# Kernel tuning notes

Measured on AMD Instinct MI355X. Metric: run time of the kernel, lower is better.

## Reference

```python
import jax, jax.numpy as jnp
import numpy as np

N_NODES = 100000


def gcn_conv(x, src, dst, w, W, b, n):
    # PyG GCNConv: add self loops (weight 1), symmetric normalization,
    # linear transform, scatter-add aggregation, bias.
    loop = jnp.arange(n, dtype=src.dtype)
    s = jnp.concatenate([src, loop])
    d = jnp.concatenate([dst, loop])
    ew = jnp.concatenate([w, jnp.ones((n,), dtype=w.dtype)])
    deg = jax.ops.segment_sum(ew, d, num_segments=n)          # [N]
    dinv = jnp.where(deg > 0, jax.lax.rsqrt(deg), 0.0).astype(x.dtype)
    norm = dinv[s] * ew * dinv[d]                             # [E+N]
    h = x @ W                                                 # [N, out]
    msg = h[s] * norm[:, None]                                # gather + scale
    out = jax.ops.segment_sum(msg, d, num_segments=n)         # scatter-add
    return out + b


def setup_inputs() -> dict:
    key = jax.random.key(0)
    k1, k2, k3, k4, k5, k6 = jax.random.split(key, 6)
    n, e, c_in, c_hid, c_out = N_NODES, 1200000, 64, 64, 32
    node_matrix = jax.random.normal(k1, (n, c_in), dtype=jnp.float32)
    edge_index = jax.random.randint(k2, (2, e), 0, n, dtype=jnp.int64)
    edge_weights = jax.random.uniform(k3, (e,), dtype=jnp.float32)
    s_in = 1.0 / np.sqrt(c_in)
    s_hid = 1.0 / np.sqrt(c_hid)
    W1 = jax.random.uniform(k4, (c_in, c_hid), jnp.float32, -s_in, s_in)
    b1 = jnp.zeros((c_hid,), jnp.float32)
    W2 = jax.random.uniform(k5, (c_hid, c_out), jnp.float32, -s_hid, s_hid)
    b2 = jnp.zeros((c_out,), jnp.float32)
    return {"node_matrix": node_matrix, "edge_index": edge_index,
            "edge_weights": edge_weights, "W1": W1, "b1": b1, "W2": W2, "b2": b2}


def reference(node_matrix, edge_index, edge_weights, W1, b1, W2, b2):
    n = node_matrix.shape[0]
    src, dst = edge_index[0], edge_index[1]
    x = gcn_conv(node_matrix, src, dst, edge_weights, W1, b1, n)
    x = jax.nn.relu(x)
    x = gcn_conv(x, src, dst, edge_weights, W2, b2, n)
    return x
```

## Files before the change

### kernel.cpp

```cpp
#include <hip/hip_runtime.h>

static inline int ceil_div(long long a, long long b) { return (int)((a + b - 1) / b); }

#define RBITS 8
#define RNODES 256
#define CNT_BLOCKS 96

typedef __attribute__((ext_vector_type(8))) short bf16x8;
typedef __attribute__((ext_vector_type(4))) float f32x4;

__device__ inline unsigned f2bf(float f) {
    unsigned u = __float_as_uint(f);
    return (u + 0x7fffu + ((u >> 16) & 1u)) >> 16;
}
__device__ inline unsigned pack2(float a, float b) { return f2bf(a) | (f2bf(b) << 16); }
__device__ inline float bf2f(unsigned v) { return __uint_as_float(v << 16); }
__device__ inline float bf_lo(unsigned v) { return __uint_as_float(v << 16); }
__device__ inline float bf_hi(unsigned v) { return __uint_as_float(v & 0xffff0000u); }

__global__ void bin_count(const int* __restrict__ dst, int* __restrict__ hist_g,
                          int NB, int E) {
    __shared__ int hist[512];
    int t = threadIdx.x;
    hist[t] = 0;
    __syncthreads();
    int nvec = E >> 2;
    const int4* d4 = (const int4*)dst;
    for (int v = blockIdx.x * 512 + t; v < nvec; v += CNT_BLOCKS * 512) {
        int4 d = d4[v];
        atomicAdd(&hist[d.x >> RBITS], 1);
        atomicAdd(&hist[d.y >> RBITS], 1);
        atomicAdd(&hist[d.z >> RBITS], 1);
        atomicAdd(&hist[d.w >> RBITS], 1);
    }
    if (blockIdx.x == 0 && t < (E & 3))
        atomicAdd(&hist[dst[(nvec << 2) + t] >> RBITS], 1);
    __syncthreads();
    if (t < NB) hist_g[blockIdx.x * NB + t] = hist[t];
}

__global__ void bin_scan(const int* __restrict__ hist_g, int* __restrict__ bin_start,
                         int* __restrict__ bin_cursor, int NB) {
    __shared__ int s[512];
    int t = threadIdx.x;
    int v = 0;
    if (t < NB) {
        for (int k = 0; k < CNT_BLOCKS; ++k) v += hist_g[k * NB + t];
        bin_cursor[t] = 0;
    }
    s[t] = v;
    __syncthreads();
    for (int d = 1; d < 512; d <<= 1) {
        int a = (t >= d) ? s[t - d] : 0;
        __syncthreads();
        s[t] += a;
        __syncthreads();
    }
    if (t < NB) bin_start[t] = s[t] - v;
    if (t == NB - 1) bin_start[NB] = s[t];
}

#define SC_T 512
#define SC_K 8
#define SC_E (SC_T * SC_K)
__global__ void bin_scatter(const int* __restrict__ src, const int* __restrict__ dst,
                            const float* __restrict__ w, int* __restrict__ bin_cursor,
                            const int* __restrict__ bin_start,
                            int* __restrict__ bp, float* __restrict__ bw,
                            int NB, int E) {
    __shared__ int hist[512];
    __shared__ int offs[512];
    __shared__ int base[512];
    __shared__ int stage_p[SC_E];
    __shared__ float stage_w[SC_E];
    __shared__ unsigned short stage_b[SC_E];
    int t = threadIdx.x;
    hist[t] = 0;
    __syncthreads();
    int e0 = blockIdx.x * SC_E;
    int nE = E - e0; if (nE > SC_E) nE = SC_E;

    int myBin[SC_K], myRank[SC_K], myPack[SC_K];
    float myW[SC_K];
#pragma unroll
    for (int k = 0; k < SC_K; ++k) {
        int idx = t + k * SC_T;
        if (idx < nE) {
            int e = e0 + idx;
            int d = dst[e];
            int b = d >> RBITS;
            myBin[k] = b;
            myPack[k] = (src[e] << RBITS) | (d & (RNODES - 1));
            myW[k] = w[e];
            myRank[k] = atomicAdd(&hist[b], 1);
        }
    }
    __syncthreads();
    offs[t] = hist[t];
    __syncthreads();
    for (int d = 1; d < 512; d <<= 1) {
        int a = (t >= d) ? offs[t - d] : 0;
        __syncthreads();
        offs[t] += a;
        __syncthreads();
    }
    if (t < NB && hist[t]) base[t] = bin_start[t] + atomicAdd(&bin_cursor[t], hist[t]);
#pragma unroll
    for (int k = 0; k < SC_K; ++k) {
        int idx = t + k * SC_T;
        if (idx < nE) {
            int b = myBin[k];
            int pos = (offs[b] - hist[b]) + myRank[k];
            stage_p[pos] = myPack[k];
            stage_w[pos] = myW[k];
            stage_b[pos] = (unsigned short)b;
        }
    }
    __syncthreads();
    for (int p = t; p < nE; p += SC_T) {
        int b = stage_b[p];
        int g = base[b] + (p - (offs[b] - hist[b]));
        bp[g] = stage_p[p];
        bw[g] = stage_w[p];
    }
}

__global__ void deg_csr(const int* __restrict__ bp, const float* __restrict__ bw,
                        const int* __restrict__ bin_start,
                        int* __restrict__ row_beg, int* __restrict__ row_cnt,
                        float* __restrict__ dinv, int N) {
    __shared__ int cnt[RNODES];
    __shared__ float wsum[RNODES];
    __shared__ int starts[RNODES];
    int b = blockIdx.x;
    int t = threadIdx.x;
    if (t < RNODES) { cnt[t] = 0; wsum[t] = 0.f; }
    __syncthreads();
    int beg = bin_start[b], end = bin_start[b + 1];
    for (int e = beg + t; e < end; e += 512) {
        int off = bp[e] & (RNODES - 1);
        atomicAdd(&cnt[off], 1);
        atomicAdd(&wsum[off], bw[e]);
    }
    __syncthreads();
    if (t < RNODES) starts[t] = cnt[t];
    __syncthreads();
    for (int d = 1; d < RNODES; d <<= 1) {
        int a = 0;
        if (t < RNODES && t >= d) a = starts[t - d];
        __syncthreads();
        if (t < RNODES) starts[t] += a;
        __syncthreads();
    }
    if (t < RNODES) {
        int node = (b << RBITS) + t;
        if (node < N) {
            row_beg[node] = beg + (starts[t] - cnt[t]);
            row_cnt[node] = cnt[t];
            dinv[node] = rsqrtf(wsum[t] + 1.0f);
        }
    }
}

__global__ void csr_scatter(const int* __restrict__ bp, const float* __restrict__ bw,
                            const int* __restrict__ bin_start, const int* __restrict__ row_beg,
                            const float* __restrict__ dinv, uint2* __restrict__ ew, int N) {
    __shared__ int cur[RNODES];
    int b = blockIdx.x;
    int t = threadIdx.x;
    if (t < RNODES) {
        int node = (b << RBITS) + t;
        cur[t] = (node < N) ? row_beg[node] : 0;
    }
    __syncthreads();
    int beg = bin_start[b], end = bin_start[b + 1];
    for (int e = beg + t; e < end; e += 512) {
        int p = bp[e];
        int s = p >> RBITS;
        int slot = atomicAdd(&cur[p & (RNODES - 1)], 1);
        uint2 v;
        v.x = (unsigned)s;
        v.y = __float_as_uint(bw[e] * dinv[s]);
        ew[slot] = v;
    }
}

__global__ __launch_bounds__(256) void gemm1_mfma(const float* __restrict__ X,
                                                  const float* __restrict__ W,
                                                  unsigned short* __restrict__ H, int N) {
    int lane = threadIdx.x & 63;
    int wv = threadIdx.x >> 6;
    int quad = lane >> 4;
    int col = lane & 15;

    bf16x8 Bh[4][2], Bl[4][2];
#pragma unroll
    for (int nt = 0; nt < 4; ++nt)
#pragma unroll
        for (int kh = 0; kh < 2; ++kh)
#pragma unroll
            for (int j = 0; j < 8; ++j) {
                float wval = W[(kh * 32 + quad * 8 + j) * 64 + nt * 16 + col];
                unsigned hb = f2bf(wval);
                Bh[nt][kh][j] = (short)hb;
                Bl[nt][kh][j] = (short)f2bf(wval - bf2f(hb));
            }

#pragma unroll
    for (int rt = 0; rt < 4; ++rt) {
        int rb = blockIdx.x * 256 + wv * 64 + rt * 16;
        if (rb >= N) break;
        int arow = rb + col;
        bf16x8 Ah[2], Al[2];
#pragma unroll
        for (int kh = 0; kh < 2; ++kh) {
            float xv[8];
            if (arow < N) {
                const float4* p = (const float4*)(X + (size_t)arow * 64 + kh * 32 + quad * 8);
                float4 f0 = p[0], f1 = p[1];
                xv[0] = f0.x; xv[1] = f0.y; xv[2] = f0.z; xv[3] = f0.w;
                xv[4] = f1.x; xv[5] = f1.y; xv[6] = f1.z; xv[7] = f1.w;
            } else {
#pragma unroll
                for (int j = 0; j < 8; ++j) xv[j] = 0.f;
            }
#pragma unroll
            for (int j = 0; j < 8; ++j) {
                unsigned hb = f2bf(xv[j]);
                Ah[kh][j] = (short)hb;
                Al[kh][j] = (short)f2bf(xv[j] - bf2f(hb));
            }
        }
        f32x4 acc[4] = {{0,0,0,0},{0,0,0,0},{0,0,0,0},{0,0,0,0}};
#pragma unroll
        for (int nt = 0; nt < 4; ++nt)
#pragma unroll
            for (int kh = 0; kh < 2; ++kh) {
                acc[nt] = __builtin_amdgcn_mfma_f32_16x16x32_bf16(Ah[kh], Bh[nt][kh], acc[nt], 0, 0, 0);
                acc[nt] = __builtin_amdgcn_mfma_f32_16x16x32_bf16(Al[kh], Bh[nt][kh], acc[nt], 0, 0, 0);
                acc[nt] = __builtin_amdgcn_mfma_f32_16x16x32_bf16(Ah[kh], Bl[nt][kh], acc[nt], 0, 0, 0);
            }
#pragma unroll
        for (int nt = 0; nt < 4; ++nt)
#pragma unroll
            for (int r = 0; r < 4; ++r) {
                int row = rb + quad * 4 + r;
                if (row < N)
                    H[(size_t)row * 64 + nt * 16 + col] = (unsigned short)f2bf(acc[nt][r]);
            }
    }
}

__global__ __launch_bounds__(256) void gemm2_mfma(const unsigned short* __restrict__ Xb,
                                                  const float* __restrict__ W,
                                                  unsigned short* __restrict__ H, int N) {
    int lane = threadIdx.x & 63;
    int wv = threadIdx.x >> 6;
    int quad = lane >> 4;
    int col = lane & 15;

    bf16x8 Bh[2][2], Bl[2][2];
#pragma unroll
    for (int nt = 0; nt < 2; ++nt)
#pragma unroll
        for (int kh = 0; kh < 2; ++kh)
#pragma unroll
            for (int j = 0; j < 8; ++j) {
                float wval = W[(kh * 32 + quad * 8 + j) * 32 + nt * 16 + col];
                unsigned hb = f2bf(wval);
                Bh[nt][kh][j] = (short)hb;
                Bl[nt][kh][j] = (short)f2bf(wval - bf2f(hb));
            }

#pragma unroll
    for (int rt = 0; rt < 4; ++rt) {
        int rb = blockIdx.x * 256 + wv * 64 + rt * 16;
        if (rb >= N) break;
        int arow = rb + col;
        bf16x8 A[2];
#pragma unroll
        for (int kh = 0; kh < 2; ++kh) {
            if (arow < N) {
                const bf16x8* p = (const bf16x8*)(Xb + (size_t)arow * 64 + kh * 32 + quad * 8);
                A[kh] = *p;
            } else {
                A[kh] = bf16x8{0,0,0,0,0,0,0,0};
            }
        }
        f32x4 acc[2] = {{0,0,0,0},{0,0,0,0}};
#pragma unroll
        for (int nt = 0; nt < 2; ++nt)
#pragma unroll
            for (int kh = 0; kh < 2; ++kh) {
                acc[nt] = __builtin_amdgcn_mfma_f32_16x16x32_bf16(A[kh], Bh[nt][kh], acc[nt], 0, 0, 0);
                acc[nt] = __builtin_amdgcn_mfma_f32_16x16x32_bf16(A[kh], Bl[nt][kh], acc[nt], 0, 0, 0);
            }
#pragma unroll
        for (int nt = 0; nt < 2; ++nt)
#pragma unroll
            for (int r = 0; r < 4; ++r) {
                int row = rb + quad * 4 + r;
                if (row < N)
                    H[(size_t)row * 32 + nt * 16 + col] = (unsigned short)f2bf(acc[nt][r]);
            }
    }
}

__global__ void aggregate64(const unsigned* __restrict__ h, const int* __restrict__ row_beg,
                            const int* __restrict__ row_cnt, const uint2* __restrict__ ew,
                            const float* __restrict__ dinv, const float* __restrict__ b,
                            unsigned* __restrict__ outb, int N) {
    int t = threadIdx.x;
    int c = t & 7;
    int i = blockIdx.x * 64 + (t >> 3);
    if (i >= N) return;
    int e = row_beg[i];
    int end = e + row_cnt[i];
    const uint4* h4 = (const uint4*)h;
    float acc[8];
#pragma unroll
    for (int j = 0; j < 8; ++j) acc[j] = 0.f;
    for (; e + 3 < end; e += 4) {
        uint2 e0 = ew[e], e1 = ew[e + 1], e2 = ew[e + 2], e3 = ew[e + 3];
        float n0 = __uint_as_float(e0.y);
        float n1 = __uint_as_float(e1.y);
        float n2 = __uint_as_float(e2.y);
        float n3 = __uint_as_float(e3.y);
        uint4 v0 = h4[(size_t)e0.x * 8 + c];
        uint4 v1 = h4[(size_t)e1.x * 8 + c];
        uint4 v2 = h4[(size_t)e2.x * 8 + c];
        uint4 v3 = h4[(size_t)e3.x * 8 + c];
        acc[0] += n0 * bf_lo(v0.x) + n1 * bf_lo(v1.x) + n2 * bf_lo(v2.x) + n3 * bf_lo(v3.x);
        acc[1] += n0 * bf_hi(v0.x) + n1 * bf_hi(v1.x) + n2 * bf_hi(v2.x) + n3 * bf_hi(v3.x);
        acc[2] += n0 * bf_lo(v0.y) + n1 * bf_lo(v1.y) + n2 * bf_lo(v2.y) + n3 * bf_lo(v3.y);
        acc[3] += n0 * bf_hi(v0.y) + n1 * bf_hi(v1.y) + n2 * bf_hi(v2.y) + n3 * bf_hi(v3.y);
        acc[4] += n0 * bf_lo(v0.z) + n1 * bf_lo(v1.z) + n2 * bf_lo(v2.z) + n3 * bf_lo(v3.z);
        acc[5] += n0 * bf_hi(v0.z) + n1 * bf_hi(v1.z) + n2 * bf_hi(v2.z) + n3 * bf_hi(v3.z);
        acc[6] += n0 * bf_lo(v0.w) + n1 * bf_lo(v1.w) + n2 * bf_lo(v2.w) + n3 * bf_lo(v3.w);
        acc[7] += n0 * bf_hi(v0.w) + n1 * bf_hi(v1.w) + n2 * bf_hi(v2.w) + n3 * bf_hi(v3.w);
    }
    for (; e < end; ++e) {
        uint2 e0 = ew[e];
        float n0 = __uint_as_float(e0.y);
        uint4 v0 = h4[(size_t)e0.x * 8 + c];
        acc[0] += n0 * bf_lo(v0.x);
        acc[1] += n0 * bf_hi(v0.x);
        acc[2] += n0 * bf_lo(v0.y);
        acc[3] += n0 * bf_hi(v0.y);
        acc[4] += n0 * bf_lo(v0.z);
        acc[5] += n0 * bf_hi(v0.z);
        acc[6] += n0 * bf_lo(v0.w);
        acc[7] += n0 * bf_hi(v0.w);
    }
    float di = dinv[i];
    uint4 hv = h4[(size_t)i * 8 + c];
    float hs[8] = {bf_lo(hv.x), bf_hi(hv.x), bf_lo(hv.y), bf_hi(hv.y),
                   bf_lo(hv.z), bf_hi(hv.z), bf_lo(hv.w), bf_hi(hv.w)};
    float4 b0 = ((const float4*)b)[c * 2];
    float4 b1 = ((const float4*)b)[c * 2 + 1];
    float o[8];
    o[0] = b0.x + di * (di * hs[0] + acc[0]);
    o[1] = b0.y + di * (di * hs[1] + acc[1]);
    o[2] = b0.z + di * (di * hs[2] + acc[2]);
    o[3] = b0.w + di * (di * hs[3] + acc[3]);
    o[4] = b1.x + di * (di * hs[4] + acc[4]);
    o[5] = b1.y + di * (di * hs[5] + acc[5]);
    o[6] = b1.z + di * (di * hs[6] + acc[6]);
    o[7] = b1.w + di * (di * hs[7] + acc[7]);
#pragma unroll
    for (int j = 0; j < 8; ++j) o[j] = fmaxf(o[j], 0.f);
    uint4 ov;
    ov.x = pack2(o[0], o[1]);
    ov.y = pack2(o[2], o[3]);
    ov.z = pack2(o[4], o[5]);
    ov.w = pack2(o[6], o[7]);
    ((uint4*)outb)[(size_t)i * 8 + c] = ov;
}

__global__ void aggregate32(const unsigned* __restrict__ h, const int* __restrict__ row_beg,
                            const int* __restrict__ row_cnt, const uint2* __restrict__ ew,
                            const float* __restrict__ dinv, const float* __restrict__ b,
                            float* __restrict__ out, int N) {
    int t = threadIdx.x;
    int c = t & 3;
    int i = blockIdx.x * 128 + (t >> 2);
    if (i >= N) return;
    int e = row_beg[i];
    int end = e + row_cnt[i];
    const uint4* h4 = (const uint4*)h;
    float acc[8];
#pragma unroll
    for (int j = 0; j < 8; ++j) acc[j] = 0.f;
    for (; e + 3 < end; e += 4) {
        uint2 e0 = ew[e], e1 = ew[e + 1], e2 = ew[e + 2], e3 = ew[e + 3];
        float n0 = __uint_as_float(e0.y);
        float n1 = __uint_as_float(e1.y);
        float n2 = __uint_as_float(e2.y);
        float n3 = __uint_as_float(e3.y);
        uint4 v0 = h4[(size_t)e0.x * 4 + c];
        uint4 v1 = h4[(size_t)e1.x * 4 + c];
        uint4 v2 = h4[(size_t)e2.x * 4 + c];
        uint4 v3 = h4[(size_t)e3.x * 4 + c];
        acc[0] += n0 * bf_lo(v0.x) + n1 * bf_lo(v1.x) + n2 * bf_lo(v2.x) + n3 * bf_lo(v3.x);
        acc[1] += n0 * bf_hi(v0.x) + n1 * bf_hi(v1.x) + n2 * bf_hi(v2.x) + n3 * bf_hi(v3.x);
        acc[2] += n0 * bf_lo(v0.y) + n1 * bf_lo(v1.y) + n2 * bf_lo(v2.y) + n3 * bf_lo(v3.y);
        acc[3] += n0 * bf_hi(v0.y) + n1 * bf_hi(v1.y) + n2 * bf_hi(v2.y) + n3 * bf_hi(v3.y);
        acc[4] += n0 * bf_lo(v0.z) + n1 * bf_lo(v1.z) + n2 * bf_lo(v2.z) + n3 * bf_lo(v3.z);
        acc[5] += n0 * bf_hi(v0.z) + n1 * bf_hi(v1.z) + n2 * bf_hi(v2.z) + n3 * bf_hi(v3.z);
        acc[6] += n0 * bf_lo(v0.w) + n1 * bf_lo(v1.w) + n2 * bf_lo(v2.w) + n3 * bf_lo(v3.w);
        acc[7] += n0 * bf_hi(v0.w) + n1 * bf_hi(v1.w) + n2 * bf_hi(v2.w) + n3 * bf_hi(v3.w);
    }
    for (; e < end; ++e) {
        uint2 e0 = ew[e];
        float n0 = __uint_as_float(e0.y);
        uint4 v0 = h4[(size_t)e0.x * 4 + c];
        acc[0] += n0 * bf_lo(v0.x);
        acc[1] += n0 * bf_hi(v0.x);
        acc[2] += n0 * bf_lo(v0.y);
        acc[3] += n0 * bf_hi(v0.y);
        acc[4] += n0 * bf_lo(v0.z);
        acc[5] += n0 * bf_hi(v0.z);
        acc[6] += n0 * bf_lo(v0.w);
        acc[7] += n0 * bf_hi(v0.w);
    }
    float di = dinv[i];
    uint4 hv = h4[(size_t)i * 4 + c];
    float hs[8] = {bf_lo(hv.x), bf_hi(hv.x), bf_lo(hv.y), bf_hi(hv.y),
                   bf_lo(hv.z), bf_hi(hv.z), bf_lo(hv.w), bf_hi(hv.w)};
    float4 b0 = ((const float4*)b)[c * 2];
    float4 b1 = ((const float4*)b)[c * 2 + 1];
    float4 o0, o1;
    o0.x = b0.x + di * (di * hs[0] + acc[0]);
    o0.y = b0.y + di * (di * hs[1] + acc[1]);
    o0.z = b0.z + di * (di * hs[2] + acc[2]);
    o0.w = b0.w + di * (di * hs[3] + acc[3]);
    o1.x = b1.x + di * (di * hs[4] + acc[4]);
    o1.y = b1.y + di * (di * hs[5] + acc[5]);
    o1.z = b1.z + di * (di * hs[6] + acc[6]);
    o1.w = b1.w + di * (di * hs[7] + acc[7]);
    float4* op = (float4*)(out + (size_t)i * 32 + c * 8);
    op[0] = o0;
    op[1] = o1;
}

extern "C" void kernel_launch(void* const* d_in, const int* in_sizes, int n_in,
                              void* d_out, int out_size, void* d_ws, size_t ws_size,
                              hipStream_t stream) {
    const float* x  = (const float*)d_in[0];
    const int* eidx = (const int*)d_in[1];
    const float* w  = (const float*)d_in[2];
    const float* W1 = (const float*)d_in[3];
    const float* b1 = (const float*)d_in[4];
    const float* W2 = (const float*)d_in[5];
    const float* b2 = (const float*)d_in[6];
    float* out = (float*)d_out;

    const int E = in_sizes[2];
    const int N = in_sizes[0] / 64;
    const int* src = eidx;
    const int* dst = eidx + E;
    const int NB = ceil_div(N, RNODES);

    char* ws = (char*)d_ws;
    size_t off = 0;
    auto alloc = [&](size_t bytes) -> void* {
        void* p = ws + off;
        off = (off + bytes + 255) & ~(size_t)255;
        return p;
    };
    int*      hist_g     = (int*)alloc((size_t)CNT_BLOCKS * NB * 4);
    int*      bin_cursor = (int*)alloc((size_t)NB * 4);
    int*      bin_start  = (int*)alloc((size_t)(NB + 1) * 4);
    int*      bp         = (int*)alloc((size_t)E * 4);
    float*    bw         = (float*)alloc((size_t)E * 4);
    uint2*    ew         = (uint2*)alloc((size_t)E * 8);
    int*      row_beg    = (int*)alloc((size_t)N * 4);
    int*      row_cnt    = (int*)alloc((size_t)N * 4);
    float*    dinv       = (float*)alloc((size_t)N * 4);
    unsigned* h1         = (unsigned*)alloc((size_t)N * 32 * 4);
    unsigned* out1b      = (unsigned*)alloc((size_t)N * 32 * 4);
    unsigned* h2         = (unsigned*)alloc((size_t)N * 16 * 4);

    bin_count<<<CNT_BLOCKS, 512, 0, stream>>>(dst, hist_g, NB, E);
    bin_scan<<<1, 512, 0, stream>>>(hist_g, bin_start, bin_cursor, NB);
    bin_scatter<<<ceil_div(E, SC_E), SC_T, 0, stream>>>(src, dst, w, bin_cursor, bin_start,
                                                        bp, bw, NB, E);
    deg_csr<<<NB, 512, 0, stream>>>(bp, bw, bin_start, row_beg, row_cnt, dinv, N);
    csr_scatter<<<NB, 512, 0, stream>>>(bp, bw, bin_start, row_beg, dinv, ew, N);

    gemm1_mfma<<<ceil_div(N, 256), 256, 0, stream>>>(x, W1, (unsigned short*)h1, N);
    aggregate64<<<ceil_div(N, 64), 512, 0, stream>>>(h1, row_beg, row_cnt, ew, dinv, b1, out1b, N);

    gemm2_mfma<<<ceil_div(N, 256), 256, 0, stream>>>((const unsigned short*)out1b, W2,
                                                     (unsigned short*)h2, N);
    aggregate32<<<ceil_div(N, 128), 512, 0, stream>>>(h2, row_beg, row_cnt, ew, dinv, b2, out, N);
}
```

Before: 203.0 us.

## Use fixed-capacity bins, fuse CSR build, fold source normalization into GEMMs

```diff
diff --git a/kernel.cpp b/kernel.cpp
--- a/kernel.cpp
+++ b/kernel.cpp
@@ -4,10 +4,13 @@
 
 #define RBITS 8
 #define RNODES 256
-#define CNT_BLOCKS 96
+#define CAPB 12
+#define CAP 4096
 
 typedef __attribute__((ext_vector_type(8))) short bf16x8;
 typedef __attribute__((ext_vector_type(4))) float f32x4;
+typedef __attribute__((ext_vector_type(2))) unsigned u32x2;
+typedef __attribute__((ext_vector_type(4))) unsigned u32x4;
 
 __device__ inline unsigned f2bf(float f) {
     unsigned u = __float_as_uint(f);
@@ -17,55 +20,12 @@
 __device__ inline float bf2f(unsigned v) { return __uint_as_float(v << 16); }
 __device__ inline float bf_lo(unsigned v) { return __uint_as_float(v << 16); }
 __device__ inline float bf_hi(unsigned v) { return __uint_as_float(v & 0xffff0000u); }
-
-__global__ void bin_count(const int* __restrict__ dst, int* __restrict__ hist_g,
-                          int NB, int E) {
-    __shared__ int hist[512];
-    int t = threadIdx.x;
-    hist[t] = 0;
-    __syncthreads();
-    int nvec = E >> 2;
-    const int4* d4 = (const int4*)dst;
-    for (int v = blockIdx.x * 512 + t; v < nvec; v += CNT_BLOCKS * 512) {
-        int4 d = d4[v];
-        atomicAdd(&hist[d.x >> RBITS], 1);
-        atomicAdd(&hist[d.y >> RBITS], 1);
-        atomicAdd(&hist[d.z >> RBITS], 1);
-        atomicAdd(&hist[d.w >> RBITS], 1);
-    }
-    if (blockIdx.x == 0 && t < (E & 3))
-        atomicAdd(&hist[dst[(nvec << 2) + t] >> RBITS], 1);
-    __syncthreads();
-    if (t < NB) hist_g[blockIdx.x * NB + t] = hist[t];
-}
-
-__global__ void bin_scan(const int* __restrict__ hist_g, int* __restrict__ bin_start,
-                         int* __restrict__ bin_cursor, int NB) {
-    __shared__ int s[512];
-    int t = threadIdx.x;
-    int v = 0;
-    if (t < NB) {
-        for (int k = 0; k < CNT_BLOCKS; ++k) v += hist_g[k * NB + t];
-        bin_cursor[t] = 0;
-    }
-    s[t] = v;
-    __syncthreads();
-    for (int d = 1; d < 512; d <<= 1) {
-        int a = (t >= d) ? s[t - d] : 0;
-        __syncthreads();
-        s[t] += a;
-        __syncthreads();
-    }
-    if (t < NB) bin_start[t] = s[t] - v;
-    if (t == NB - 1) bin_start[NB] = s[t];
-}
 
 #define SC_T 512
 #define SC_K 8
 #define SC_E (SC_T * SC_K)
 __global__ void bin_scatter(const int* __restrict__ src, const int* __restrict__ dst,
                             const float* __restrict__ w, int* __restrict__ bin_cursor,
-                            const int* __restrict__ bin_start,
                             int* __restrict__ bp, float* __restrict__ bw,
                             int NB, int E) {
     __shared__ int hist[512];
@@ -104,7 +64,7 @@
         offs[t] += a;
         __syncthreads();
     }
-    if (t < NB && hist[t]) base[t] = bin_start[t] + atomicAdd(&bin_cursor[t], hist[t]);
+    if (t < NB && hist[t]) base[t] = (t << CAPB) + atomicAdd(&bin_cursor[t], hist[t]);
 #pragma unroll
     for (int k = 0; k < SC_K; ++k) {
         int idx = t + k * SC_T;
@@ -125,22 +85,29 @@
     }
 }
 
-__global__ void deg_csr(const int* __restrict__ bp, const float* __restrict__ bw,
-                        const int* __restrict__ bin_start,
-                        int* __restrict__ row_beg, int* __restrict__ row_cnt,
-                        float* __restrict__ dinv, int N) {
+__global__ void build_csr(const int* __restrict__ bp, const float* __restrict__ bw,
+                          const int* __restrict__ bin_len,
+                          unsigned* __restrict__ row_rc, float* __restrict__ dinv,
+                          u32x2* __restrict__ ew, int N) {
+    __shared__ int bp_s[CAP];
+    __shared__ float bw_s[CAP];
     __shared__ int cnt[RNODES];
     __shared__ float wsum[RNODES];
     __shared__ int starts[RNODES];
+    __shared__ int cur[RNODES];
     int b = blockIdx.x;
     int t = threadIdx.x;
+    int len = bin_len[b];
+    int base = b << CAPB;
     if (t < RNODES) { cnt[t] = 0; wsum[t] = 0.f; }
     __syncthreads();
-    int beg = bin_start[b], end = bin_start[b + 1];
-    for (int e = beg + t; e < end; e += 512) {
-        int off = bp[e] & (RNODES - 1);
-        atomicAdd(&cnt[off], 1);
-        atomicAdd(&wsum[off], bw[e]);
+    for (int e = t; e < len; e += 512) {
+        int p = bp[base + e];
+        float wv = bw[base + e];
+        bp_s[e] = p;
+        bw_s[e] = wv;
+        atomicAdd(&cnt[p & (RNODES - 1)], 1);
+        atomicAdd(&wsum[p & (RNODES - 1)], wv);
     }
     __syncthreads();
     if (t < RNODES) starts[t] = cnt[t];
@@ -153,40 +120,28 @@
         __syncthreads();
     }
     if (t < RNODES) {
+        int s0 = starts[t] - cnt[t];
+        cur[t] = s0;
         int node = (b << RBITS) + t;
         if (node < N) {
-            row_beg[node] = beg + (starts[t] - cnt[t]);
-            row_cnt[node] = cnt[t];
+            row_rc[node] = (unsigned)(base + s0) | ((unsigned)cnt[t] << 21);
             dinv[node] = rsqrtf(wsum[t] + 1.0f);
         }
     }
-}
-
-__global__ void csr_scatter(const int* __restrict__ bp, const float* __restrict__ bw,
-                            const int* __restrict__ bin_start, const int* __restrict__ row_beg,
-                            const float* __restrict__ dinv, uint2* __restrict__ ew, int N) {
-    __shared__ int cur[RNODES];
-    int b = blockIdx.x;
-    int t = threadIdx.x;
-    if (t < RNODES) {
-        int node = (b << RBITS) + t;
-        cur[t] = (node < N) ? row_beg[node] : 0;
-    }
-    __syncthreads();
-    int beg = bin_start[b], end = bin_start[b + 1];
-    for (int e = beg + t; e < end; e += 512) {
-        int p = bp[e];
-        int s = p >> RBITS;
+    __syncthreads();
+    for (int e = t; e < len; e += 512) {
+        int p = bp_s[e];
         int slot = atomicAdd(&cur[p & (RNODES - 1)], 1);
-        uint2 v;
-        v.x = (unsigned)s;
-        v.y = __float_as_uint(bw[e] * dinv[s]);
-        ew[slot] = v;
+        u32x2 v;
+        v.x = (unsigned)(p >> RBITS);
+        v.y = __float_as_uint(bw_s[e]);
+        ew[base + slot] = v;
     }
 }
 
 __global__ __launch_bounds__(256) void gemm1_mfma(const float* __restrict__ X,
                                                   const float* __restrict__ W,
+                                                  const float* __restrict__ dinv,
                                                   unsigned short* __restrict__ H, int N) {
     int lane = threadIdx.x & 63;
     int wv = threadIdx.x >> 6;
@@ -240,19 +195,26 @@
                 acc[nt] = __builtin_amdgcn_mfma_f32_16x16x32_bf16(Al[kh], Bh[nt][kh], acc[nt], 0, 0, 0);
                 acc[nt] = __builtin_amdgcn_mfma_f32_16x16x32_bf16(Ah[kh], Bl[nt][kh], acc[nt], 0, 0, 0);
             }
+        float di[4];
+#pragma unroll
+        for (int r = 0; r < 4; ++r) {
+            int row = rb + quad * 4 + r;
+            di[r] = (row < N) ? dinv[row] : 0.f;
+        }
 #pragma unroll
         for (int nt = 0; nt < 4; ++nt)
 #pragma unroll
             for (int r = 0; r < 4; ++r) {
                 int row = rb + quad * 4 + r;
                 if (row < N)
-                    H[(size_t)row * 64 + nt * 16 + col] = (unsigned short)f2bf(acc[nt][r]);
+                    H[(size_t)row * 64 + nt * 16 + col] = (unsigned short)f2bf(di[r] * acc[nt][r]);
             }
     }
 }
 
 __global__ __launch_bounds__(256) void gemm2_mfma(const unsigned short* __restrict__ Xb,
                                                   const float* __restrict__ W,
+                                                  const float* __restrict__ dinv,
                                                   unsigned short* __restrict__ H, int N) {
     int lane = threadIdx.x & 63;
     int wv = threadIdx.x >> 6;
@@ -295,33 +257,42 @@
                 acc[nt] = __builtin_amdgcn_mfma_f32_16x16x32_bf16(A[kh], Bh[nt][kh], acc[nt], 0, 0, 0);
                 acc[nt] = __builtin_amdgcn_mfma_f32_16x16x32_bf16(A[kh], Bl[nt][kh], acc[nt], 0, 0, 0);
             }
+        float di[4];
+#pragma unroll
+        for (int r = 0; r < 4; ++r) {
+            int row = rb + quad * 4 + r;
+            di[r] = (row < N) ? dinv[row] : 0.f;
+        }
 #pragma unroll
         for (int nt = 0; nt < 2; ++nt)
 #pragma unroll
             for (int r = 0; r < 4; ++r) {
                 int row = rb + quad * 4 + r;
                 if (row < N)
-                    H[(size_t)row * 32 + nt * 16 + col] = (unsigned short)f2bf(acc[nt][r]);
-            }
-    }
-}
-
-__global__ void aggregate64(const unsigned* __restrict__ h, const int* __restrict__ row_beg,
-                            const int* __restrict__ row_cnt, const uint2* __restrict__ ew,
-                            const float* __restrict__ dinv, const float* __restrict__ b,
-                            unsigned* __restrict__ outb, int N) {
+                    H[(size_t)row * 32 + nt * 16 + col] = (unsigned short)f2bf(di[r] * acc[nt][r]);
+            }
+    }
+}
+
+__global__ void aggregate64(const unsigned* __restrict__ h, const unsigned* __restrict__ row_rc,
+                            const u32x2* __restrict__ ew, const float* __restrict__ dinv,
+                            const float* __restrict__ b, unsigned* __restrict__ outb, int N) {
     int t = threadIdx.x;
     int c = t & 7;
     int i = blockIdx.x * 64 + (t >> 3);
     if (i >= N) return;
-    int e = row_beg[i];
-    int end = e + row_cnt[i];
+    unsigned rc = row_rc[i];
+    int e = (int)(rc & 0x1FFFFFu);
+    int end = e + (int)(rc >> 21);
     const uint4* h4 = (const uint4*)h;
     float acc[8];
 #pragma unroll
     for (int j = 0; j < 8; ++j) acc[j] = 0.f;
     for (; e + 3 < end; e += 4) {
-        uint2 e0 = ew[e], e1 = ew[e + 1], e2 = ew[e + 2], e3 = ew[e + 3];
+        u32x2 e0 = __builtin_nontemporal_load(&ew[e]);
+        u32x2 e1 = __builtin_nontemporal_load(&ew[e + 1]);
+        u32x2 e2 = __builtin_nontemporal_load(&ew[e + 2]);
+        u32x2 e3 = __builtin_nontemporal_load(&ew[e + 3]);
         float n0 = __uint_as_float(e0.y);
         float n1 = __uint_as_float(e1.y);
         float n2 = __uint_as_float(e2.y);
@@ -340,7 +311,7 @@
         acc[7] += n0 * bf_hi(v0.w) + n1 * bf_hi(v1.w) + n2 * bf_hi(v2.w) + n3 * bf_hi(v3.w);
     }
     for (; e < end; ++e) {
-        uint2 e0 = ew[e];
+        u32x2 e0 = __builtin_nontemporal_load(&ew[e]);
         float n0 = __uint_as_float(e0.y);
         uint4 v0 = h4[(size_t)e0.x * 8 + c];
         acc[0] += n0 * bf_lo(v0.x);
@@ -359,40 +330,43 @@
     float4 b0 = ((const float4*)b)[c * 2];
     float4 b1 = ((const float4*)b)[c * 2 + 1];
     float o[8];
-    o[0] = b0.x + di * (di * hs[0] + acc[0]);
-    o[1] = b0.y + di * (di * hs[1] + acc[1]);
-    o[2] = b0.z + di * (di * hs[2] + acc[2]);
-    o[3] = b0.w + di * (di * hs[3] + acc[3]);
-    o[4] = b1.x + di * (di * hs[4] + acc[4]);
-    o[5] = b1.y + di * (di * hs[5] + acc[5]);
-    o[6] = b1.z + di * (di * hs[6] + acc[6]);
-    o[7] = b1.w + di * (di * hs[7] + acc[7]);
+    o[0] = b0.x + di * (hs[0] + acc[0]);
+    o[1] = b0.y + di * (hs[1] + acc[1]);
+    o[2] = b0.z + di * (hs[2] + acc[2]);
+    o[3] = b0.w + di * (hs[3] + acc[3]);
+    o[4] = b1.x + di * (hs[4] + acc[4]);
+    o[5] = b1.y + di * (hs[5] + acc[5]);
+    o[6] = b1.z + di * (hs[6] + acc[6]);
+    o[7] = b1.w + di * (hs[7] + acc[7]);
 #pragma unroll
     for (int j = 0; j < 8; ++j) o[j] = fmaxf(o[j], 0.f);
-    uint4 ov;
+    u32x4 ov;
     ov.x = pack2(o[0], o[1]);
     ov.y = pack2(o[2], o[3]);
     ov.z = pack2(o[4], o[5]);
     ov.w = pack2(o[6], o[7]);
-    ((uint4*)outb)[(size_t)i * 8 + c] = ov;
-}
-
-__global__ void aggregate32(const unsigned* __restrict__ h, const int* __restrict__ row_beg,
-                            const int* __restrict__ row_cnt, const uint2* __restrict__ ew,
-                            const float* __restrict__ dinv, const float* __restrict__ b,
-                            float* __restrict__ out, int N) {
+    __builtin_nontemporal_store(ov, (u32x4*)outb + (size_t)i * 8 + c);
+}
+
+__global__ void aggregate32(const unsigned* __restrict__ h, const unsigned* __restrict__ row_rc,
+                            const u32x2* __restrict__ ew, const float* __restrict__ dinv,
+                            const float* __restrict__ b, float* __restrict__ out, int N) {
     int t = threadIdx.x;
     int c = t & 3;
     int i = blockIdx.x * 128 + (t >> 2);
     if (i >= N) return;
-    int e = row_beg[i];
-    int end = e + row_cnt[i];
+    unsigned rc = row_rc[i];
+    int e = (int)(rc & 0x1FFFFFu);
+    int end = e + (int)(rc >> 21);
     const uint4* h4 = (const uint4*)h;
     float acc[8];
 #pragma unroll
     for (int j = 0; j < 8; ++j) acc[j] = 0.f;
     for (; e + 3 < end; e += 4) {
-        uint2 e0 = ew[e], e1 = ew[e + 1], e2 = ew[e + 2], e3 = ew[e + 3];
+        u32x2 e0 = __builtin_nontemporal_load(&ew[e]);
+        u32x2 e1 = __builtin_nontemporal_load(&ew[e + 1]);
+        u32x2 e2 = __builtin_nontemporal_load(&ew[e + 2]);
+        u32x2 e3 = __builtin_nontemporal_load(&ew[e + 3]);
         float n0 = __uint_as_float(e0.y);
         float n1 = __uint_as_float(e1.y);
         float n2 = __uint_as_float(e2.y);
@@ -411,7 +385,7 @@
         acc[7] += n0 * bf_hi(v0.w) + n1 * bf_hi(v1.w) + n2 * bf_hi(v2.w) + n3 * bf_hi(v3.w);
     }
     for (; e < end; ++e) {
-        uint2 e0 = ew[e];
+        u32x2 e0 = __builtin_nontemporal_load(&ew[e]);
         float n0 = __uint_as_float(e0.y);
         uint4 v0 = h4[(size_t)e0.x * 4 + c];
         acc[0] += n0 * bf_lo(v0.x);
@@ -429,18 +403,18 @@
                    bf_lo(hv.z), bf_hi(hv.z), bf_lo(hv.w), bf_hi(hv.w)};
     float4 b0 = ((const float4*)b)[c * 2];
     float4 b1 = ((const float4*)b)[c * 2 + 1];
-    float4 o0, o1;
-    o0.x = b0.x + di * (di * hs[0] + acc[0]);
-    o0.y = b0.y + di * (di * hs[1] + acc[1]);
-    o0.z = b0.z + di * (di * hs[2] + acc[2]);
-    o0.w = b0.w + di * (di * hs[3] + acc[3]);
-    o1.x = b1.x + di * (di * hs[4] + acc[4]);
-    o1.y = b1.y + di * (di * hs[5] + acc[5]);
-    o1.z = b1.z + di * (di * hs[6] + acc[6]);
-    o1.w = b1.w + di * (di * hs[7] + acc[7]);
-    float4* op = (float4*)(out + (size_t)i * 32 + c * 8);
-    op[0] = o0;
-    op[1] = o1;
+    f32x4 o0, o1;
+    o0.x = b0.x + di * (hs[0] + acc[0]);
+    o0.y = b0.y + di * (hs[1] + acc[1]);
+    o0.z = b0.z + di * (hs[2] + acc[2]);
+    o0.w = b0.w + di * (hs[3] + acc[3]);
+    o1.x = b1.x + di * (hs[4] + acc[4]);
+    o1.y = b1.y + di * (hs[5] + acc[5]);
+    o1.z = b1.z + di * (hs[6] + acc[6]);
+    o1.w = b1.w + di * (hs[7] + acc[7]);
+    f32x4* op = (f32x4*)(out + (size_t)i * 32 + c * 8);
+    __builtin_nontemporal_store(o0, op);
+    __builtin_nontemporal_store(o1, op + 1);
 }
 
 extern "C" void kernel_launch(void* const* d_in, const int* in_sizes, int n_in,
@@ -468,30 +442,24 @@
         off = (off + bytes + 255) & ~(size_t)255;
         return p;
     };
-    int*      hist_g     = (int*)alloc((size_t)CNT_BLOCKS * NB * 4);
     int*      bin_cursor = (int*)alloc((size_t)NB * 4);
-    int*      bin_start  = (int*)alloc((size_t)(NB + 1) * 4);
-    int*      bp         = (int*)alloc((size_t)E * 4);
-    float*    bw         = (float*)alloc((size_t)E * 4);
-    uint2*    ew         = (uint2*)alloc((size_t)E * 8);
-    int*      row_beg    = (int*)alloc((size_t)N * 4);
-    int*      row_cnt    = (int*)alloc((size_t)N * 4);
+    int*      bp         = (int*)alloc((size_t)NB * CAP * 4);
+    float*    bw         = (float*)alloc((size_t)NB * CAP * 4);
+    u32x2*    ew         = (u32x2*)alloc((size_t)NB * CAP * 8);
+    unsigned* row_rc     = (unsigned*)alloc((size_t)N * 4);
     float*    dinv       = (float*)alloc((size_t)N * 4);
     unsigned* h1         = (unsigned*)alloc((size_t)N * 32 * 4);
     unsigned* out1b      = (unsigned*)alloc((size_t)N * 32 * 4);
     unsigned* h2         = (unsigned*)alloc((size_t)N * 16 * 4);
 
-    bin_count<<<CNT_BLOCKS, 512, 0, stream>>>(dst, hist_g, NB, E);
-    bin_scan<<<1, 512, 0, stream>>>(hist_g, bin_start, bin_cursor, NB);
-    bin_scatter<<<ceil_div(E, SC_E), SC_T, 0, stream>>>(src, dst, w, bin_cursor, bin_start,
-                                                        bp, bw, NB, E);
-    deg_csr<<<NB, 512, 0, stream>>>(bp, bw, bin_start, row_beg, row_cnt, dinv, N);
-    csr_scatter<<<NB, 512, 0, stream>>>(bp, bw, bin_start, row_beg, dinv, ew, N);
-
-    gemm1_mfma<<<ceil_div(N, 256), 256, 0, stream>>>(x, W1, (unsigned short*)h1, N);
-    aggregate64<<<ceil_div(N, 64), 512, 0, stream>>>(h1, row_beg, row_cnt, ew, dinv, b1, out1b, N);
-
-    gemm2_mfma<<<ceil_div(N, 256), 256, 0, stream>>>((const unsigned short*)out1b, W2,
+    (void)hipMemsetAsync(bin_cursor, 0, (size_t)NB * 4, stream);
+    bin_scatter<<<ceil_div(E, SC_E), SC_T, 0, stream>>>(src, dst, w, bin_cursor, bp, bw, NB, E);
+    build_csr<<<NB, 512, 0, stream>>>(bp, bw, bin_cursor, row_rc, dinv, ew, N);
+
+    gemm1_mfma<<<ceil_div(N, 256), 256, 0, stream>>>(x, W1, dinv, (unsigned short*)h1, N);
+    aggregate64<<<ceil_div(N, 64), 512, 0, stream>>>(h1, row_rc, ew, dinv, b1, out1b, N);
+
+    gemm2_mfma<<<ceil_div(N, 256), 256, 0, stream>>>((const unsigned short*)out1b, W2, dinv,
                                                      (unsigned short*)h2, N);
-    aggregate32<<<ceil_div(N, 128), 512, 0, stream>>>(h2, row_beg, row_cnt, ew, dinv, b2, out, N);
-}
+    aggregate32<<<ceil_div(N, 128), 512, 0, stream>>>(h2, row_rc, ew, dinv, b2, out, N);
+}
```

Measured after the change: 213.0 us. +4.9%, slower.
